# Kernel optimization log

Hardware: AMD Instinct MI355X
Metric: run time of the kernel (lower is better)

The kernel has to match this reference:

```python
import jax, jax.numpy as jnp
import numpy as np

EPS = 1e-3  # Keras LayerNormalization default epsilon


def layernorm(x, g, b):
    mu = jnp.mean(x, axis=-1, keepdims=True)
    var = jnp.var(x, axis=-1, keepdims=True)
    return (x - mu) * jax.lax.rsqrt(var + EPS) * g + b


def setup_inputs() -> dict:
    key = jax.random.key(0)
    ks = jax.random.split(key, 16)
    B, T, C = 2, 2048, 1024
    F = 4 * C
    std = 0.02
    inp = {
        "x": jax.random.normal(ks[0], (B, T, C), jnp.float32),
        "ln1_g": jnp.ones((C,), jnp.float32),
        "ln1_b": jnp.zeros((C,), jnp.float32),
        "Wq": std * jax.random.normal(ks[1], (C, C), jnp.float32),
        "bq": jnp.zeros((C,), jnp.float32),
        "Wk": std * jax.random.normal(ks[2], (C, C), jnp.float32),
        "bk": jnp.zeros((C,), jnp.float32),
        "Wv": std * jax.random.normal(ks[3], (C, C), jnp.float32),
        "bv": jnp.zeros((C,), jnp.float32),
        "ln2_g": jnp.ones((C,), jnp.float32),
        "ln2_b": jnp.zeros((C,), jnp.float32),
        "W1": std * jax.random.normal(ks[4], (C, F), jnp.float32),
        "b1": jnp.zeros((F,), jnp.float32),
        "W2": std * jax.random.normal(ks[5], (F, C), jnp.float32),
        "b2": jnp.zeros((C,), jnp.float32),
    }
    return inp


N_HEADS = 16


def reference(x, ln1_g, ln1_b, Wq, bq, Wk, bk, Wv, bv, ln2_g, ln2_b, W1, b1, W2, b2):
    B, T, C = x.shape
    H = N_HEADS
    D = C // H

    h = layernorm(x, ln1_g, ln1_b)
    # [B,T,C] -> [B,H,T,D]
    def split_heads(y):
        return y.reshape(B, T, H, D).transpose(0, 2, 1, 3)

    q = split_heads(h @ Wq + bq)
    k = split_heads(h @ Wk + bk)
    v = split_heads(h @ Wv + bv)

    # Faithful to original: scores = K @ Q^T, i.e. scores[i,j] = k_i . q_j
    scores = jnp.einsum("bhid,bhjd->bhij", k, q) / jnp.sqrt(jnp.float32(D))
    causal = jnp.tril(jnp.ones((T, T), bool))  # [T,T]
    scores = jnp.where(causal[None, None], scores, -jnp.inf)
    w = jax.nn.softmax(scores, axis=-1)
    attn = jnp.einsum("bhij,bhjd->bhid", w, v)  # [B,H,T,D]
    attn = attn.transpose(0, 2, 1, 3).reshape(B, T, C)
    x = x + attn

    h2 = layernorm(x, ln2_g, ln2_b)
    ffn = jax.nn.gelu(h2 @ W1 + b1, approximate=False) @ W2 + b2
    x = x + ffn
    return x
```

## Files before the change

kernel.cpp:

```cpp
#include <hip/hip_runtime.h>
#include <hip/hip_bf16.h>
#include <math.h>

typedef __hip_bfloat16 bf16;
typedef __attribute__((ext_vector_type(8))) short bf16x8;
typedef __attribute__((ext_vector_type(4))) float f32x4;

__device__ __forceinline__ unsigned short f2bf_rne(float f) {
  unsigned u = __float_as_uint(f);
  u += 0x7fffu + ((u >> 16) & 1u);
  return (unsigned short)(u >> 16);
}
__device__ __forceinline__ float bf2f(unsigned short s) {
  return __uint_as_float(((unsigned)s) << 16);
}

__device__ __forceinline__ float gelu_fast(float v) {
  float u = v * (0.7978845608f + 0.0356774081f * v * v);
  float t = __builtin_amdgcn_exp2f(u * 2.8853900818f);
  float r = __builtin_amdgcn_rcpf(t + 1.0f);
  return v - v * r;
}

#define GLOBAL_AS __attribute__((address_space(1)))
#define LDS_AS __attribute__((address_space(3)))
__device__ __forceinline__ void gl2lds16(const void* g, void* l) {
  __builtin_amdgcn_global_load_lds((const GLOBAL_AS void*)g, (LDS_AS void*)l, 16, 0, 0);
}

__global__ __launch_bounds__(256) void ln_kernel(const float* __restrict__ x,
                                                 const float* __restrict__ g,
                                                 const float* __restrict__ b,
                                                 bf16* __restrict__ h) {
  int row = blockIdx.x, t = threadIdx.x;
  const float4 xv = ((const float4*)(x + (size_t)row * 1024))[t];
  float s = xv.x + xv.y + xv.z + xv.w;
  float sq = xv.x * xv.x + xv.y * xv.y + xv.z * xv.z + xv.w * xv.w;
  #pragma unroll
  for (int m = 1; m < 64; m <<= 1) { s += __shfl_xor(s, m); sq += __shfl_xor(sq, m); }
  __shared__ float ps[4], pq[4];
  if ((t & 63) == 0) { ps[t >> 6] = s; pq[t >> 6] = sq; }
  __syncthreads();
  s = ps[0] + ps[1] + ps[2] + ps[3];
  sq = pq[0] + pq[1] + pq[2] + pq[3];
  float mean = s * (1.0f / 1024.0f);
  float var = sq * (1.0f / 1024.0f) - mean * mean;
  float rs = rsqrtf(var + 1e-3f);
  float4 gv = ((const float4*)g)[t];
  float4 bv = ((const float4*)b)[t];
  ushort4 o;
  o.x = f2bf_rne((xv.x - mean) * rs * gv.x + bv.x);
  o.y = f2bf_rne((xv.y - mean) * rs * gv.y + bv.y);
  o.z = f2bf_rne((xv.z - mean) * rs * gv.z + bv.z);
  o.w = f2bf_rne((xv.w - mean) * rs * gv.w + bv.w);
  ((ushort4*)(h + (size_t)row * 1024))[t] = o;
}

__device__ __forceinline__ void tr_tile(const float* __restrict__ W, bf16* __restrict__ WT,
                                        int R, int Cc, int bx, int by, int t) {
  __shared__ float tile[32][33];
  int tx = t & 31, ty = t >> 5;
  #pragma unroll
  for (int k = 0; k < 4; k++) {
    int rr = ty + k * 8;
    tile[rr][tx] = W[(size_t)(by + rr) * Cc + bx + tx];
  }
  __syncthreads();
  unsigned short* out = reinterpret_cast<unsigned short*>(WT);
  #pragma unroll
  for (int k = 0; k < 4; k++) {
    int rr = ty + k * 8;
    out[(size_t)(bx + rr) * R + by + tx] = f2bf_rne(tile[tx][rr]);
  }
}

__global__ __launch_bounds__(256) void transpose_all(const float* __restrict__ Wq,
                                                     const float* __restrict__ Wk,
                                                     const float* __restrict__ Wv,
                                                     const float* __restrict__ W1,
                                                     const float* __restrict__ W2,
                                                     bf16* __restrict__ WqkT,
                                                     bf16* __restrict__ W1T,
                                                     bf16* __restrict__ W2T) {
  int id = blockIdx.x, t = threadIdx.x;
  if (id < 3072) {
    int sect = id >> 10, r = id & 1023;
    const float* W = sect == 0 ? Wq : (sect == 1 ? Wk : Wv);
    bf16* WT = WqkT + (size_t)sect * 1048576;
    tr_tile(W, WT, 1024, 1024, (r & 31) * 32, (r >> 5) * 32, t);
  } else if (id < 7168) {
    int r = id - 3072;
    tr_tile(W1, W1T, 1024, 4096, (r & 127) * 32, (r >> 7) * 32, t);
  } else {
    int r = id - 7168;
    tr_tile(W2, W2T, 4096, 1024, (r & 31) * 32, (r >> 5) * 32, t);
  }
}

__device__ __forceinline__ void mainloop_256(const bf16* __restrict__ A,
                                             const bf16* __restrict__ BT,
                                             int lda, int nk, int m0, int n0,
                                             char* ldsb, int t,
                                             f32x4 (&acc)[8][4]) {
  const int lane = t & 63, wave = t >> 6;
  const int l = lane & 15, quad = lane >> 4;
  const int wm = (wave >> 2) * 128, wn = (wave & 3) * 64;
  const int srow = wave * 8 + (lane >> 3);
  const int scol = ((lane & 7) ^ (lane >> 3)) * 8;
  const int grp0 = (quad ^ (l & 7)) * 16;
  const int grp1 = ((4 + quad) ^ (l & 7)) * 16;

  bf16x8 a[4][2], b01[2][2], b23[2][2];

  auto stA = [&](int buf, int half, int kt) {
    const bf16* s = A + (size_t)(m0 + half * 128 + srow) * lda + kt * 64 + scol;
    char* d = ldsb + buf * 65536 + half * 16384 + wave * 1024;
    gl2lds16(s, d);
    gl2lds16(s + (size_t)64 * lda, d + 8192);
  };
  auto stB = [&](int buf, int half, int kt) {
    const bf16* s = BT + (size_t)(n0 + half * 128 + srow) * lda + kt * 64 + scol;
    char* d = ldsb + buf * 65536 + 32768 + half * 16384 + wave * 1024;
    gl2lds16(s, d);
    gl2lds16(s + (size_t)64 * lda, d + 8192);
  };
  auto rdA = [&](int buf, int mh) {
    const char* base = ldsb + buf * 65536 + (wm + mh * 64 + l) * 128;
    #pragma unroll
    for (int ii = 0; ii < 4; ii++) {
      a[ii][0] = *(const bf16x8*)(base + ii * 2048 + grp0);
      a[ii][1] = *(const bf16x8*)(base + ii * 2048 + grp1);
    }
  };
  auto rdB = [&](int buf, int nh, bf16x8 (&bb)[2][2]) {
    const char* base = ldsb + buf * 65536 + 32768 + (wn + nh * 32 + l) * 128;
    #pragma unroll
    for (int jj = 0; jj < 2; jj++) {
      bb[jj][0] = *(const bf16x8*)(base + jj * 2048 + grp0);
      bb[jj][1] = *(const bf16x8*)(base + jj * 2048 + grp1);
    }
  };
  auto mm4 = [&](int mi, bf16x8 (&bb)[2][2], int nj) {
    #pragma unroll
    for (int ii = 0; ii < 4; ii++)
      #pragma unroll
      for (int jj = 0; jj < 2; jj++) {
        acc[mi + ii][nj + jj] = __builtin_amdgcn_mfma_f32_16x16x32_bf16(
            a[ii][0], bb[jj][0], acc[mi + ii][nj + jj], 0, 0, 0);
        acc[mi + ii][nj + jj] = __builtin_amdgcn_mfma_f32_16x16x32_bf16(
            a[ii][1], bb[jj][1], acc[mi + ii][nj + jj], 0, 0, 0);
      }
  };

#define BARX() __builtin_amdgcn_s_barrier()
#define LGKM0() do { asm volatile("s_waitcnt lgkmcnt(0)" ::: "memory"); \
                     __builtin_amdgcn_sched_barrier(0); } while (0)
#define HALF4(BC, DOA, SAB, SAK, DOB, SBB, SBK, VMN)                      \
  do {                                                                    \
    rdA(BC, 0); rdB(BC, 0, b01);                                          \
    if (DOA) stA(SAB, 0, SAK);                                            \
    BARX(); LGKM0();                                                      \
    __builtin_amdgcn_s_setprio(1); mm4(0, b01, 0);                        \
    __builtin_amdgcn_s_setprio(0); BARX();                                \
    rdB(BC, 1, b23);                                                      \
    if (DOA) stA(SAB, 1, SAK);                                            \
    BARX(); LGKM0();                                                      \
    __builtin_amdgcn_s_setprio(1); mm4(0, b23, 2);                        \
    __builtin_amdgcn_s_setprio(0); BARX();                                \
    rdA(BC, 1);                                                           \
    if (DOB) stB(SBB, 0, SBK);                                            \
    BARX(); LGKM0();                                                      \
    __builtin_amdgcn_s_setprio(1); mm4(4, b01, 0);                        \
    __builtin_amdgcn_s_setprio(0); BARX();                                \
    if (DOB) stB(SBB, 1, SBK);                                            \
    BARX();                                                               \
    __builtin_amdgcn_s_setprio(1); mm4(4, b23, 2);                        \
    __builtin_amdgcn_s_setprio(0);                                        \
    asm volatile("s_waitcnt vmcnt(" VMN ")" ::: "memory");                \
    BARX();                                                               \
  } while (0)

  const int nt = nk >> 6;
  stA(0, 0, 0); stA(0, 1, 0);
  stB(0, 0, 0); stB(0, 1, 0);
  stB(1, 0, 1); stB(1, 1, 1);
  asm volatile("s_waitcnt vmcnt(4)" ::: "memory");
  BARX();
  int tt = 0;
  for (; tt + 2 < nt; tt += 2) {
    HALF4(0, 1, 1, tt + 1, 1, 0, tt + 2, "4");
    HALF4(1, 1, 0, tt + 2, 1, 1, tt + 3, "4");
  }
  HALF4(0, 1, 1, tt + 1, 0, 0, 0, "0");
  HALF4(1, 0, 0, 0, 0, 0, 0, "0");
#undef HALF4
#undef LGKM0
#undef BARX
}

__global__ __launch_bounds__(512, 2) void gemm_ffn1(const bf16* __restrict__ A,
                                                    const bf16* __restrict__ BT,
                                                    const float* __restrict__ bias,
                                                    bf16* __restrict__ out,
                                                    int N, int K) {
  extern __shared__ char lds[];
  int t = threadIdx.x;
  int n0 = blockIdx.x * 256, m0 = blockIdx.y * 256;
  f32x4 acc[8][4];
  #pragma unroll
  for (int i = 0; i < 8; i++)
    #pragma unroll
    for (int j = 0; j < 4; j++) acc[i][j] = (f32x4){0.f, 0.f, 0.f, 0.f};
  mainloop_256(A, BT, K, K, m0, n0, lds, t, acc);

  int lane = t & 63, wave = t >> 6;
  int l = lane & 15, quad = lane >> 4;
  int wm = (wave >> 2) * 128, wn = (wave & 3) * 64;
  int r4 = quad * 4;
  unsigned short* os = reinterpret_cast<unsigned short*>(out);
  #pragma unroll
  for (int i = 0; i < 8; i++)
    #pragma unroll
    for (int j = 0; j < 4; j++) {
      int col = n0 + wn + j * 16 + l;
      float bval = bias[col];
      #pragma unroll
      for (int r = 0; r < 4; r++) {
        int row = m0 + wm + i * 16 + r4 + r;
        os[(size_t)row * N + col] = f2bf_rne(gelu_fast(acc[i][j][r] + bval));
      }
    }
}

__global__ __launch_bounds__(512, 2) void gemm_ffn2(const bf16* __restrict__ A,
                                                    const bf16* __restrict__ BT,
                                                    unsigned short* __restrict__ p0,
                                                    unsigned short* __restrict__ p1,
                                                    unsigned short* __restrict__ p2,
                                                    unsigned short* __restrict__ p3) {
  extern __shared__ char lds[];
  int t = threadIdx.x;
  int n0 = blockIdx.x * 256, m0 = blockIdx.y * 256;
  int z = blockIdx.z;
  f32x4 acc[8][4];
  #pragma unroll
  for (int i = 0; i < 8; i++)
    #pragma unroll
    for (int j = 0; j < 4; j++) acc[i][j] = (f32x4){0.f, 0.f, 0.f, 0.f};
  mainloop_256(A + z * 1024, BT + z * 1024, 4096, 1024, m0, n0, lds, t, acc);

  unsigned short* p = z == 0 ? p0 : (z == 1 ? p1 : (z == 2 ? p2 : p3));
  int lane = t & 63, wave = t >> 6;
  int l = lane & 15, quad = lane >> 4;
  int wm = (wave >> 2) * 128, wn = (wave & 3) * 64;
  int r4 = quad * 4;
  #pragma unroll
  for (int i = 0; i < 8; i++)
    #pragma unroll
    for (int j = 0; j < 4; j++) {
      int col = n0 + wn + j * 16 + l;
      #pragma unroll
      for (int r = 0; r < 4; r++) {
        int row = m0 + wm + i * 16 + r4 + r;
        p[(size_t)row * 1024 + col] = f2bf_rne(acc[i][j][r]);
      }
    }
}

__global__ __launch_bounds__(256) void reduce_ffn2(const unsigned short* __restrict__ p0,
                                                   const unsigned short* __restrict__ p1,
                                                   const unsigned short* __restrict__ p2,
                                                   const unsigned short* __restrict__ p3,
                                                   const float* __restrict__ x1,
                                                   const float* __restrict__ bias,
                                                   float* __restrict__ out) {
  int row = blockIdx.x, t = threadIdx.x;
  size_t base = (size_t)row * 1024;
  ushort4 a = ((const ushort4*)(p0 + base))[t];
  ushort4 b = ((const ushort4*)(p1 + base))[t];
  ushort4 c = ((const ushort4*)(p2 + base))[t];
  ushort4 d = ((const ushort4*)(p3 + base))[t];
  float4 xv = ((const float4*)(x1 + base))[t];
  float4 bv = ((const float4*)bias)[t];
  float4 o;
  o.x = (bf2f(a.x) + bf2f(b.x)) + (bf2f(c.x) + bf2f(d.x)) + xv.x + bv.x;
  o.y = (bf2f(a.y) + bf2f(b.y)) + (bf2f(c.y) + bf2f(d.y)) + xv.y + bv.y;
  o.z = (bf2f(a.z) + bf2f(b.z)) + (bf2f(c.z) + bf2f(d.z)) + xv.z + bv.z;
  o.w = (bf2f(a.w) + bf2f(b.w)) + (bf2f(c.w) + bf2f(d.w)) + xv.w + bv.w;
  ((float4*)(out + base))[t] = o;
}

__global__ __launch_bounds__(512, 2) void gemm_qkv(const bf16* __restrict__ A,
                                                   const bf16* __restrict__ BT,
                                                   const float* __restrict__ bq,
                                                   const float* __restrict__ bk,
                                                   const float* __restrict__ bv,
                                                   bf16* __restrict__ qb,
                                                   bf16* __restrict__ kb,
                                                   bf16* __restrict__ vt,
                                                   int K) {
  extern __shared__ char lds[];
  int t = threadIdx.x;
  int n0 = blockIdx.x * 256, m0 = blockIdx.y * 256;
  f32x4 acc[8][4];
  #pragma unroll
  for (int i = 0; i < 8; i++)
    #pragma unroll
    for (int j = 0; j < 4; j++) acc[i][j] = (f32x4){0.f, 0.f, 0.f, 0.f};
  mainloop_256(A, BT, K, K, m0, n0, lds, t, acc);

  int lane = t & 63, wave = t >> 6;
  int l = lane & 15, quad = lane >> 4;
  int wm = (wave >> 2) * 128, wn = (wave & 3) * 64;
  int sect = n0 >> 10;
  const float* bias = sect == 0 ? bq : (sect == 1 ? bk : bv);
  int r4 = quad * 4;
  #pragma unroll
  for (int i = 0; i < 8; i++)
    #pragma unroll
    for (int j = 0; j < 4; j++) {
      int col = n0 + wn + j * 16 + l;
      int c1 = col & 1023;
      float bval = bias[c1];
      int row0 = m0 + wm + i * 16 + r4;
      if (sect < 2) {
        bf16* o = sect == 0 ? qb : kb;
        unsigned short* os = reinterpret_cast<unsigned short*>(o);
        #pragma unroll
        for (int r = 0; r < 4; r++)
          os[(size_t)(row0 + r) * 1024 + c1] = f2bf_rne(acc[i][j][r] + bval);
      } else {
        int hh = c1 >> 6, d = c1 & 63;
        int b = row0 >> 11, t0 = row0 & 2047;
        ushort4 pk;
        pk.x = f2bf_rne(acc[i][j][0] + bval);
        pk.y = f2bf_rne(acc[i][j][1] + bval);
        pk.z = f2bf_rne(acc[i][j][2] + bval);
        pk.w = f2bf_rne(acc[i][j][3] + bval);
        *(ushort4*)((unsigned short*)vt + (size_t)((b * 16 + hh) * 64 + d) * 2048 + t0) = pk;
      }
    }
}

__global__ __launch_bounds__(256, 4) void attn_mfma(const bf16* __restrict__ qb,
                                                    const bf16* __restrict__ kb,
                                                    const bf16* __restrict__ vt,
                                                    const float* __restrict__ x,
                                                    float* __restrict__ x1) {
  __shared__ bf16 QP[64][64];
  __shared__ bf16 KV[2][2][64][64];
  int t = threadIdx.x;
  int bh = blockIdx.x;
  int b = bh >> 4, h = bh & 15;
  size_t qk_base = (size_t)b * 2048 * 1024 + (size_t)h * 64;
  size_t vt_base = (size_t)bh * 64 * 2048;
  int lane = t & 63, wave = t >> 6;
  int l = lane & 15, quad = lane >> 4;
  int sw = l & 7;
  int srow8 = lane >> 3;
  int scol = ((lane & 7) ^ srow8) * 8;
  const float cs = 0.125f * 1.44269504088896f;
  int y = blockIdx.y;
  int yr = y & 7, yk = y >> 3;
  int it = yk == 0 ? 31 - yr : (yk == 1 ? 16 + yr : (yk == 2 ? 15 - yr : yr));
  int i0 = it * 64;
  int njt = it + 1;
  int iblk = i0 + wave * 16;

  #pragma unroll
  for (int c = 0; c < 2; c++) {
    int rr = wave * 16 + c * 8 + srow8;
    gl2lds16(kb + qk_base + (size_t)(i0 + rr) * 1024 + scol,
             (char*)QP + wave * 2048 + c * 1024);
    gl2lds16(qb + qk_base + (size_t)rr * 1024 + scol,
             (char*)KV + wave * 2048 + c * 1024);
    gl2lds16(vt + vt_base + (size_t)rr * 2048 + scol,
             (char*)KV + 8192 + wave * 2048 + c * 1024);
  }
  __syncthreads();

  const char* qr = (const char*)&QP[wave * 16 + l][0];
  bf16x8 qf0 = *(const bf16x8*)(qr + ((quad ^ sw) * 16));
  bf16x8 qf1 = *(const bf16x8*)(qr + (((4 + quad) ^ sw) * 16));
  float lsum = 0.f;
  f32x4 Oacc[4];
  #pragma unroll
  for (int dt = 0; dt < 4; dt++) Oacc[dt] = (f32x4){0.f, 0.f, 0.f, 0.f};

  char* Pw = (char*)&QP[wave * 16 + l][0];

  int buf = 0;
  for (int jt = 0; jt < njt; jt++) {
    int j0v = jt * 64;
    if (jt + 1 < njt) {
      int j1 = j0v + 64;
      #pragma unroll
      for (int c = 0; c < 2; c++) {
        int rr = wave * 16 + c * 8 + srow8;
        gl2lds16(qb + qk_base + (size_t)(j1 + rr) * 1024 + scol,
                 (char*)KV + (buf ^ 1) * 16384 + wave * 2048 + c * 1024);
        gl2lds16(vt + vt_base + (size_t)rr * 2048 + j1 + scol,
                 (char*)KV + (buf ^ 1) * 16384 + 8192 + wave * 2048 + c * 1024);
      }
    }

    const bf16* Kb = &KV[buf][0][0][0];
    #pragma unroll
    for (int nt = 0; nt < 4; nt++) {
      int jb = j0v + nt * 16;
      uint2 pk;
      if (jb > iblk + 15) {
        pk.x = 0u; pk.y = 0u;
      } else {
        const bf16* kr = Kb + (nt * 16 + l) * 64;
        bf16x8 kf0 = *(const bf16x8*)(kr + ((quad ^ sw) * 8));
        bf16x8 kf1 = *(const bf16x8*)(kr + (((4 + quad) ^ sw) * 8));
        f32x4 sv = (f32x4){0.f, 0.f, 0.f, 0.f};
        sv = __builtin_amdgcn_mfma_f32_16x16x32_bf16(kf0, qf0, sv, 0, 0, 0);
        sv = __builtin_amdgcn_mfma_f32_16x16x32_bf16(kf1, qf1, sv, 0, 0, 0);
        float p0, p1, p2, p3;
        if (jb + 15 <= iblk) {
          p0 = __builtin_amdgcn_exp2f(sv[0] * cs);
          p1 = __builtin_amdgcn_exp2f(sv[1] * cs);
          p2 = __builtin_amdgcn_exp2f(sv[2] * cs);
          p3 = __builtin_amdgcn_exp2f(sv[3] * cs);
        } else {
          int i_ = iblk + l, jbase = jb + quad * 4;
          p0 = (jbase + 0 > i_) ? 0.f : __builtin_amdgcn_exp2f(sv[0] * cs);
          p1 = (jbase + 1 > i_) ? 0.f : __builtin_amdgcn_exp2f(sv[1] * cs);
          p2 = (jbase + 2 > i_) ? 0.f : __builtin_amdgcn_exp2f(sv[2] * cs);
          p3 = (jbase + 3 > i_) ? 0.f : __builtin_amdgcn_exp2f(sv[3] * cs);
        }
        lsum += (p0 + p1) + (p2 + p3);
        union { __hip_bfloat162 h2; unsigned u; } c0u, c1u;
        c0u.h2 = __float22bfloat162_rn(make_float2(p0, p1));
        c1u.h2 = __float22bfloat162_rn(make_float2(p2, p3));
        pk.x = c0u.u; pk.y = c1u.u;
      }
      *(uint2*)(Pw + (((nt * 2 + (quad >> 1)) ^ sw) << 4) + ((quad & 1) << 3)) = pk;
    }
    asm volatile("s_waitcnt lgkmcnt(0)" ::: "memory");

    bf16x8 ap0 = *(const bf16x8*)(Pw + ((quad ^ sw) << 4));
    bf16x8 ap1 = *(const bf16x8*)(Pw + (((4 + quad) ^ sw) << 4));
    const bf16* Vb = &KV[buf][1][0][0];
    #pragma unroll
    for (int dt = 0; dt < 4; dt++) {
      const bf16* vr = Vb + (dt * 16 + l) * 64;
      bf16x8 bv0 = *(const bf16x8*)(vr + ((quad ^ sw) * 8));
      bf16x8 bv1 = *(const bf16x8*)(vr + (((4 + quad) ^ sw) * 8));
      Oacc[dt] = __builtin_amdgcn_mfma_f32_16x16x32_bf16(ap0, bv0, Oacc[dt], 0, 0, 0);
      Oacc[dt] = __builtin_amdgcn_mfma_f32_16x16x32_bf16(ap1, bv1, Oacc[dt], 0, 0, 0);
    }
    __syncthreads();
    buf ^= 1;
  }

  lsum += __shfl_xor(lsum, 16);
  lsum += __shfl_xor(lsum, 32);
  #pragma unroll
  for (int r = 0; r < 4; r++) {
    float lv = __shfl(lsum, quad * 4 + r);
    float inv = 1.0f / lv;
    int row = iblk + quad * 4 + r;
    size_t gi = qk_base + (size_t)row * 1024;
    #pragma unroll
    for (int dt = 0; dt < 4; dt++) {
      int d = dt * 16 + l;
      x1[gi + d] = x[gi + d] + Oacc[dt][r] * inv;
    }
  }
}

extern "C" void kernel_launch(void* const* d_in, const int* in_sizes, int n_in,
                              void* d_out, int out_size, void* d_ws, size_t ws_size,
                              hipStream_t stream) {
  const float* x    = (const float*)d_in[0];
  const float* ln1g = (const float*)d_in[1];
  const float* ln1b = (const float*)d_in[2];
  const float* Wq   = (const float*)d_in[3];
  const float* bq   = (const float*)d_in[4];
  const float* Wk   = (const float*)d_in[5];
  const float* bk   = (const float*)d_in[6];
  const float* Wv   = (const float*)d_in[7];
  const float* bv   = (const float*)d_in[8];
  const float* ln2g = (const float*)d_in[9];
  const float* ln2b = (const float*)d_in[10];
  const float* W1   = (const float*)d_in[11];
  const float* b1   = (const float*)d_in[12];
  const float* W2   = (const float*)d_in[13];
  const float* b2   = (const float*)d_in[14];

  char* ws = (char*)d_ws;
  float* x1  = (float*)(ws + 0);
  bf16* h    = (bf16*)(ws + 16777216);
  bf16* WqkT = (bf16*)(ws + 25165824);
  bf16* W1T  = (bf16*)(ws + 31457280);
  bf16* W2T  = (bf16*)(ws + 39845888);
  bf16* qb   = (bf16*)(ws + 48234496);
  bf16* kb   = (bf16*)(ws + 56623104);
  bf16* vt   = (bf16*)(ws + 65011712);
  bf16* act  = (bf16*)(ws + 73400320);

  static bool s_attr_done = false;
  if (!s_attr_done) {
    hipFuncSetAttribute(reinterpret_cast<const void*>(gemm_qkv),
                        hipFuncAttributeMaxDynamicSharedMemorySize, 131072);
    hipFuncSetAttribute(reinterpret_cast<const void*>(gemm_ffn1),
                        hipFuncAttributeMaxDynamicSharedMemorySize, 131072);
    hipFuncSetAttribute(reinterpret_cast<const void*>(gemm_ffn2),
                        hipFuncAttributeMaxDynamicSharedMemorySize, 131072);
    s_attr_done = true;
  }

  transpose_all<<<11264, 256, 0, stream>>>(Wq, Wk, Wv, W1, W2, WqkT, W1T, W2T);
  ln_kernel<<<4096, 256, 0, stream>>>(x, ln1g, ln1b, h);
  gemm_qkv<<<dim3(12, 16), 512, 131072, stream>>>(h, WqkT, bq, bk, bv, qb, kb, vt, 1024);
  attn_mfma<<<dim3(32, 32), 256, 0, stream>>>(qb, kb, vt, x, x1);
  ln_kernel<<<4096, 256, 0, stream>>>(x1, ln2g, ln2b, h);
  gemm_ffn1<<<dim3(16, 16), 512, 131072, stream>>>(h, W1T, b1, act, 4096, 1024);
  gemm_ffn2<<<dim3(4, 16, 4), 512, 131072, stream>>>(act, W2T,
      (unsigned short*)qb, (unsigned short*)kb, (unsigned short*)vt, (unsigned short*)h);
  reduce_ffn2<<<4096, 256, 0, stream>>>((const unsigned short*)qb, (const unsigned short*)kb,
                                        (const unsigned short*)vt, (const unsigned short*)h,
                                        x1, b2, (float*)d_out);
}
```

Measured before the change: 295.9 us.

## Split attention key tiles across two wave groups and reduce partial outputs in LDS

The attention kernel now runs 512 threads per block, split into two groups of four waves. Each group processes alternating 64-wide key/value tiles with its own double buffer in dynamic LDS. The two partial output accumulators and row sums are combined through shared memory at the end. The block-to-query-tile mapping is also simplified to a straight reverse order instead of the interleaved order. The goal is to halve the serial key loop per block and cut the tail on long causal rows, at the cost of larger LDS use (80KB), fewer resident blocks, and an extra reduction step.

```diff
diff --git a/kernel.cpp b/kernel.cpp
--- a/kernel.cpp
+++ b/kernel.cpp
@@ -342,132 +342,167 @@
     }
 }
 
-__global__ __launch_bounds__(256, 4) void attn_mfma(const bf16* __restrict__ qb,
+__global__ __launch_bounds__(512, 4) void attn_mfma(const bf16* __restrict__ qb,
                                                     const bf16* __restrict__ kb,
                                                     const bf16* __restrict__ vt,
                                                     const float* __restrict__ x,
                                                     float* __restrict__ x1) {
-  __shared__ bf16 QP[64][64];
-  __shared__ bf16 KV[2][2][64][64];
+  extern __shared__ char alds[];
+  char* KVb = alds;
+  char* Pb  = alds + 65536;
   int t = threadIdx.x;
   int bh = blockIdx.x;
   int b = bh >> 4, h = bh & 15;
   size_t qk_base = (size_t)b * 2048 * 1024 + (size_t)h * 64;
   size_t vt_base = (size_t)bh * 64 * 2048;
   int lane = t & 63, wave = t >> 6;
+  int g = wave >> 2, w4 = wave & 3;
   int l = lane & 15, quad = lane >> 4;
   int sw = l & 7;
   int srow8 = lane >> 3;
   int scol = ((lane & 7) ^ srow8) * 8;
   const float cs = 0.125f * 1.44269504088896f;
-  int y = blockIdx.y;
-  int yr = y & 7, yk = y >> 3;
-  int it = yk == 0 ? 31 - yr : (yk == 1 ? 16 + yr : (yk == 2 ? 15 - yr : yr));
+  int it = 31 - blockIdx.y;
   int i0 = it * 64;
   int njt = it + 1;
-  int iblk = i0 + wave * 16;
-
-  #pragma unroll
-  for (int c = 0; c < 2; c++) {
-    int rr = wave * 16 + c * 8 + srow8;
-    gl2lds16(kb + qk_base + (size_t)(i0 + rr) * 1024 + scol,
-             (char*)QP + wave * 2048 + c * 1024);
-    gl2lds16(qb + qk_base + (size_t)rr * 1024 + scol,
-             (char*)KV + wave * 2048 + c * 1024);
-    gl2lds16(vt + vt_base + (size_t)rr * 2048 + scol,
-             (char*)KV + 8192 + wave * 2048 + c * 1024);
+  int iblk = i0 + w4 * 16;
+
+  if (g == 0) {
+    #pragma unroll
+    for (int c = 0; c < 2; c++) {
+      int rr = w4 * 16 + c * 8 + srow8;
+      gl2lds16(kb + qk_base + (size_t)(i0 + rr) * 1024 + scol,
+               Pb + w4 * 2048 + c * 1024);
+      gl2lds16(qb + qk_base + (size_t)rr * 1024 + scol,
+               KVb + w4 * 2048 + c * 1024);
+      gl2lds16(vt + vt_base + (size_t)rr * 2048 + scol,
+               KVb + 8192 + w4 * 2048 + c * 1024);
+    }
+  } else if (njt > 1) {
+    #pragma unroll
+    for (int c = 0; c < 2; c++) {
+      int rr = w4 * 16 + c * 8 + srow8;
+      gl2lds16(qb + qk_base + (size_t)(64 + rr) * 1024 + scol,
+               KVb + 32768 + w4 * 2048 + c * 1024);
+      gl2lds16(vt + vt_base + (size_t)rr * 2048 + 64 + scol,
+               KVb + 32768 + 8192 + w4 * 2048 + c * 1024);
+    }
   }
   __syncthreads();
 
-  const char* qr = (const char*)&QP[wave * 16 + l][0];
+  const char* qr = Pb + w4 * 2048 + l * 128;
   bf16x8 qf0 = *(const bf16x8*)(qr + ((quad ^ sw) * 16));
   bf16x8 qf1 = *(const bf16x8*)(qr + (((4 + quad) ^ sw) * 16));
+  __syncthreads();
+
   float lsum = 0.f;
   f32x4 Oacc[4];
   #pragma unroll
   for (int dt = 0; dt < 4; dt++) Oacc[dt] = (f32x4){0.f, 0.f, 0.f, 0.f};
 
-  char* Pw = (char*)&QP[wave * 16 + l][0];
-
+  char* Pw = Pb + wave * 2048 + l * 128;
+  char* KVg = KVb + g * 32768;
+  int nstep = (njt + 1) >> 1;
   int buf = 0;
-  for (int jt = 0; jt < njt; jt++) {
-    int j0v = jt * 64;
-    if (jt + 1 < njt) {
-      int j1 = j0v + 64;
+  for (int s = 0; s < nstep; s++) {
+    int jt = 2 * s + g;
+    if (jt + 2 < njt) {
+      int j1 = (jt + 2) * 64;
       #pragma unroll
       for (int c = 0; c < 2; c++) {
-        int rr = wave * 16 + c * 8 + srow8;
+        int rr = w4 * 16 + c * 8 + srow8;
         gl2lds16(qb + qk_base + (size_t)(j1 + rr) * 1024 + scol,
-                 (char*)KV + (buf ^ 1) * 16384 + wave * 2048 + c * 1024);
+                 KVg + (buf ^ 1) * 16384 + w4 * 2048 + c * 1024);
         gl2lds16(vt + vt_base + (size_t)rr * 2048 + j1 + scol,
-                 (char*)KV + (buf ^ 1) * 16384 + 8192 + wave * 2048 + c * 1024);
-      }
-    }
-
-    const bf16* Kb = &KV[buf][0][0][0];
-    #pragma unroll
-    for (int nt = 0; nt < 4; nt++) {
-      int jb = j0v + nt * 16;
-      uint2 pk;
-      if (jb > iblk + 15) {
-        pk.x = 0u; pk.y = 0u;
-      } else {
-        const bf16* kr = Kb + (nt * 16 + l) * 64;
-        bf16x8 kf0 = *(const bf16x8*)(kr + ((quad ^ sw) * 8));
-        bf16x8 kf1 = *(const bf16x8*)(kr + (((4 + quad) ^ sw) * 8));
-        f32x4 sv = (f32x4){0.f, 0.f, 0.f, 0.f};
-        sv = __builtin_amdgcn_mfma_f32_16x16x32_bf16(kf0, qf0, sv, 0, 0, 0);
-        sv = __builtin_amdgcn_mfma_f32_16x16x32_bf16(kf1, qf1, sv, 0, 0, 0);
-        float p0, p1, p2, p3;
-        if (jb + 15 <= iblk) {
-          p0 = __builtin_amdgcn_exp2f(sv[0] * cs);
-          p1 = __builtin_amdgcn_exp2f(sv[1] * cs);
-          p2 = __builtin_amdgcn_exp2f(sv[2] * cs);
-          p3 = __builtin_amdgcn_exp2f(sv[3] * cs);
+                 KVg + (buf ^ 1) * 16384 + 8192 + w4 * 2048 + c * 1024);
+      }
+    }
+    if (jt < njt) {
+      int j0v = jt * 64;
+      const bf16* Kb = (const bf16*)(KVg + buf * 16384);
+      #pragma unroll
+      for (int nt = 0; nt < 4; nt++) {
+        int jb = j0v + nt * 16;
+        uint2 pk;
+        if (jb > iblk + 15) {
+          pk.x = 0u; pk.y = 0u;
         } else {
-          int i_ = iblk + l, jbase = jb + quad * 4;
-          p0 = (jbase + 0 > i_) ? 0.f : __builtin_amdgcn_exp2f(sv[0] * cs);
-          p1 = (jbase + 1 > i_) ? 0.f : __builtin_amdgcn_exp2f(sv[1] * cs);
-          p2 = (jbase + 2 > i_) ? 0.f : __builtin_amdgcn_exp2f(sv[2] * cs);
-          p3 = (jbase + 3 > i_) ? 0.f : __builtin_amdgcn_exp2f(sv[3] * cs);
+          const bf16* kr = Kb + (nt * 16 + l) * 64;
+          bf16x8 kf0 = *(const bf16x8*)(kr + ((quad ^ sw) * 8));
+          bf16x8 kf1 = *(const bf16x8*)(kr + (((4 + quad) ^ sw) * 8));
+          f32x4 sv = (f32x4){0.f, 0.f, 0.f, 0.f};
+          sv = __builtin_amdgcn_mfma_f32_16x16x32_bf16(kf0, qf0, sv, 0, 0, 0);
+          sv = __builtin_amdgcn_mfma_f32_16x16x32_bf16(kf1, qf1, sv, 0, 0, 0);
+          float p0, p1, p2, p3;
+          if (jb + 15 <= iblk) {
+            p0 = __builtin_amdgcn_exp2f(sv[0] * cs);
+            p1 = __builtin_amdgcn_exp2f(sv[1] * cs);
+            p2 = __builtin_amdgcn_exp2f(sv[2] * cs);
+            p3 = __builtin_amdgcn_exp2f(sv[3] * cs);
+          } else {
+            int i_ = iblk + l, jbase = jb + quad * 4;
+            p0 = (jbase + 0 > i_) ? 0.f : __builtin_amdgcn_exp2f(sv[0] * cs);
+            p1 = (jbase + 1 > i_) ? 0.f : __builtin_amdgcn_exp2f(sv[1] * cs);
+            p2 = (jbase + 2 > i_) ? 0.f : __builtin_amdgcn_exp2f(sv[2] * cs);
+            p3 = (jbase + 3 > i_) ? 0.f : __builtin_amdgcn_exp2f(sv[3] * cs);
+          }
+          lsum += (p0 + p1) + (p2 + p3);
+          union { __hip_bfloat162 h2; unsigned u; } c0u, c1u;
+          c0u.h2 = __float22bfloat162_rn(make_float2(p0, p1));
+          c1u.h2 = __float22bfloat162_rn(make_float2(p2, p3));
+          pk.x = c0u.u; pk.y = c1u.u;
         }
-        lsum += (p0 + p1) + (p2 + p3);
-        union { __hip_bfloat162 h2; unsigned u; } c0u, c1u;
-        c0u.h2 = __float22bfloat162_rn(make_float2(p0, p1));
-        c1u.h2 = __float22bfloat162_rn(make_float2(p2, p3));
-        pk.x = c0u.u; pk.y = c1u.u;
-      }
-      *(uint2*)(Pw + (((nt * 2 + (quad >> 1)) ^ sw) << 4) + ((quad & 1) << 3)) = pk;
-    }
-    asm volatile("s_waitcnt lgkmcnt(0)" ::: "memory");
-
-    bf16x8 ap0 = *(const bf16x8*)(Pw + ((quad ^ sw) << 4));
-    bf16x8 ap1 = *(const bf16x8*)(Pw + (((4 + quad) ^ sw) << 4));
-    const bf16* Vb = &KV[buf][1][0][0];
-    #pragma unroll
-    for (int dt = 0; dt < 4; dt++) {
-      const bf16* vr = Vb + (dt * 16 + l) * 64;
-      bf16x8 bv0 = *(const bf16x8*)(vr + ((quad ^ sw) * 8));
-      bf16x8 bv1 = *(const bf16x8*)(vr + (((4 + quad) ^ sw) * 8));
-      Oacc[dt] = __builtin_amdgcn_mfma_f32_16x16x32_bf16(ap0, bv0, Oacc[dt], 0, 0, 0);
-      Oacc[dt] = __builtin_amdgcn_mfma_f32_16x16x32_bf16(ap1, bv1, Oacc[dt], 0, 0, 0);
+        *(uint2*)(Pw + (((nt * 2 + (quad >> 1)) ^ sw) << 4) + ((quad & 1) << 3)) = pk;
+      }
+      asm volatile("s_waitcnt lgkmcnt(0)" ::: "memory");
+
+      bf16x8 ap0 = *(const bf16x8*)(Pw + ((quad ^ sw) << 4));
+      bf16x8 ap1 = *(const bf16x8*)(Pw + (((4 + quad) ^ sw) << 4));
+      const bf16* Vb = (const bf16*)(KVg + buf * 16384 + 8192);
+      #pragma unroll
+      for (int dt = 0; dt < 4; dt++) {
+        const bf16* vr = Vb + (dt * 16 + l) * 64;
+        bf16x8 bv0 = *(const bf16x8*)(vr + ((quad ^ sw) * 8));
+        bf16x8 bv1 = *(const bf16x8*)(vr + (((4 + quad) ^ sw) * 8));
+        Oacc[dt] = __builtin_amdgcn_mfma_f32_16x16x32_bf16(ap0, bv0, Oacc[dt], 0, 0, 0);
+        Oacc[dt] = __builtin_amdgcn_mfma_f32_16x16x32_bf16(ap1, bv1, Oacc[dt], 0, 0, 0);
+      }
     }
     __syncthreads();
     buf ^= 1;
   }
 
-  lsum += __shfl_xor(lsum, 16);
-  lsum += __shfl_xor(lsum, 32);
-  #pragma unroll
-  for (int r = 0; r < 4; r++) {
-    float lv = __shfl(lsum, quad * 4 + r);
-    float inv = 1.0f / lv;
-    int row = iblk + quad * 4 + r;
-    size_t gi = qk_base + (size_t)row * 1024;
-    #pragma unroll
-    for (int dt = 0; dt < 4; dt++) {
-      int d = dt * 16 + l;
-      x1[gi + d] = x[gi + d] + Oacc[dt][r] * inv;
+  float* F = (float*)KVb;
+  int fbase = w4 * 1088;
+  if (g == 1) {
+    #pragma unroll
+    for (int dt = 0; dt < 4; dt++)
+      #pragma unroll
+      for (int r = 0; r < 4; r++)
+        F[fbase + (dt * 4 + r) * 64 + lane] = Oacc[dt][r];
+    F[fbase + 1024 + lane] = lsum;
+  }
+  __syncthreads();
+  if (g == 0) {
+    #pragma unroll
+    for (int dt = 0; dt < 4; dt++)
+      #pragma unroll
+      for (int r = 0; r < 4; r++)
+        Oacc[dt][r] += F[fbase + (dt * 4 + r) * 64 + lane];
+    lsum += F[fbase + 1024 + lane];
+    lsum += __shfl_xor(lsum, 16);
+    lsum += __shfl_xor(lsum, 32);
+    #pragma unroll
+    for (int r = 0; r < 4; r++) {
+      float lv = __shfl(lsum, quad * 4 + r);
+      float inv = 1.0f / lv;
+      int row = iblk + quad * 4 + r;
+      size_t gi = qk_base + (size_t)row * 1024;
+      #pragma unroll
+      for (int dt = 0; dt < 4; dt++) {
+        int d = dt * 16 + l;
+        x1[gi + d] = x[gi + d] + Oacc[dt][r] * inv;
+      }
     }
   }
 }
@@ -510,13 +545,15 @@
                         hipFuncAttributeMaxDynamicSharedMemorySize, 131072);
     hipFuncSetAttribute(reinterpret_cast<const void*>(gemm_ffn2),
                         hipFuncAttributeMaxDynamicSharedMemorySize, 131072);
+    hipFuncSetAttribute(reinterpret_cast<const void*>(attn_mfma),
+                        hipFuncAttributeMaxDynamicSharedMemorySize, 81920);
     s_attr_done = true;
   }
 
   transpose_all<<<11264, 256, 0, stream>>>(Wq, Wk, Wv, W1, W2, WqkT, W1T, W2T);
   ln_kernel<<<4096, 256, 0, stream>>>(x, ln1g, ln1b, h);
   gemm_qkv<<<dim3(12, 16), 512, 131072, stream>>>(h, WqkT, bq, bk, bv, qb, kb, vt, 1024);
-  attn_mfma<<<dim3(32, 32), 256, 0, stream>>>(qb, kb, vt, x, x1);
+  attn_mfma<<<dim3(32, 32), 512, 81920, stream>>>(qb, kb, vt, x, x1);
   ln_kernel<<<4096, 256, 0, stream>>>(x1, ln2g, ln2b, h);
   gemm_ffn1<<<dim3(16, 16), 512, 131072, stream>>>(h, W1T, b1, act, 4096, 1024);
   gemm_ffn2<<<dim3(4, 16, 4), 512, 131072, stream>>>(act, W2T,
```

Result: faster. 289.8 us (-2.1%).
